# Performance work log

Hardware: AMD Instinct MI355X
Metric: run time of the kernel (lower is better)

The kernel has to match this reference:

```python
import jax, jax.numpy as jnp
import numpy as np

B, C, H, W = 2, 192, 128, 128
NUM_HEADS = 6
AMP = 1
NUM_OFFSETS = 9


def bilinear_sample(img, grid):
    # img: (C, H, W); grid: (Hn, Wn, 2) in [-1,1], align_corners=True, zeros padding
    Hh, Ww = img.shape[1], img.shape[2]
    x = (grid[..., 0] + 1.0) * 0.5 * (Ww - 1)
    y = (grid[..., 1] + 1.0) * 0.5 * (Hh - 1)
    x0 = jnp.floor(x)
    y0 = jnp.floor(y)
    x1 = x0 + 1.0
    y1 = y0 + 1.0
    wx1 = x - x0
    wy1 = y - y0

    def gather(yi, xi):
        valid = ((xi >= 0) & (xi <= Ww - 1) & (yi >= 0) & (yi <= Hh - 1)).astype(img.dtype)
        xc = jnp.clip(xi, 0, Ww - 1).astype(jnp.int32)
        yc = jnp.clip(yi, 0, Hh - 1).astype(jnp.int32)
        return img[:, yc, xc] * valid  # (C, Hn, Wn)

    return (gather(y0, x0) * ((1 - wy1) * (1 - wx1))
            + gather(y0, x1) * ((1 - wy1) * wx1)
            + gather(y1, x0) * (wy1 * (1 - wx1))
            + gather(y1, x1) * (wy1 * wx1))


def setup_inputs() -> dict:
    key = jax.random.key(0)
    ks = jax.random.split(key, 8)
    s = 0.02
    Ch = C // NUM_HEADS
    return {
        "x_q": jax.random.normal(ks[0], (B, C, H, W), jnp.float32),
        "x_kv": jax.random.normal(ks[1], (B, C, H, W), jnp.float32),
        "w_q": jax.random.normal(ks[2], (C, C), jnp.float32) * s,
        "w_kv": jax.random.normal(ks[3], (2 * C, C), jnp.float32) * s,
        "w_off1": jax.random.normal(ks[4], (C, 2 * C, 3, 3), jnp.float32) * s,
        "b_off1": jnp.zeros((C,), jnp.float32),
        "w_off2": jax.random.normal(ks[5], (2 * NUM_OFFSETS, C), jnp.float32) * s,
        "b_off2": jnp.zeros((2 * NUM_OFFSETS,), jnp.float32),
        "w_proj": jax.random.normal(ks[6], (C, C), jnp.float32) * s,
        "b_proj": jnp.zeros((C,), jnp.float32),
    }


def reference(x_q, x_kv, w_q, w_kv, w_off1, b_off1, w_off2, b_off2, w_proj, b_proj):
    Ch = C // NUM_HEADS
    scale = Ch ** (-0.5)

    # 1x1 conv projections as channel matmuls
    q = jnp.einsum('oc,bchw->bohw', w_q, x_q) * scale
    kv = jnp.einsum('oc,bchw->bohw', w_kv, x_kv)
    k, v = kv[:, :C], kv[:, C:]  # kv.reshape(B,2,Ch,nh,H,W) -> first C channels are k

    # offset predictor: 3x3 conv -> relu -> 1x1 conv
    off_in = jnp.concatenate([x_q, x_kv], axis=1)
    h1 = jax.lax.conv_general_dilated(off_in, w_off1, (1, 1), 'SAME',
                                      dimension_numbers=('NCHW', 'OIHW', 'NCHW'))
    h1 = jax.nn.relu(h1 + b_off1[None, :, None, None])
    off = jnp.einsum('oc,bchw->bohw', w_off2, h1) + b_off2[None, :, None, None]
    off = off.reshape(B, NUM_OFFSETS, 2, H, W).transpose(0, 1, 3, 4, 2)  # (B,9,H,W,2)
    gx = off[..., 0] / (W - 1) * 2.0 - 1.0
    gy = off[..., 1] / (H - 1) * 2.0 - 1.0
    grid = jnp.stack([gx, gy], axis=-1)  # (B,9,H,W,2)

    # deformable gather: sample full-channel k/v at each of 9 per-pixel offset grids
    sample = jax.vmap(jax.vmap(bilinear_sample, in_axes=(None, 0)), in_axes=(0, 0))
    k_s = sample(k, grid).reshape(B, NUM_OFFSETS, Ch, NUM_HEADS, H, W)
    v_s = sample(v, grid).reshape(B, NUM_OFFSETS, Ch, NUM_HEADS, H, W)

    q = q.reshape(B, Ch, NUM_HEADS, H, W)

    pad = [(0, 0), (0, 0), (0, 0), (0, 0), (AMP, AMP), (AMP, AMP)]
    k_p = jnp.pad(k_s, pad)
    v_p = jnp.pad(v_s, pad)

    win = 2 * AMP + 1
    logits = []
    for i in range(win):
        for j in range(win):
            idx = i * win + j
            kp = k_p[:, idx, :, :, i:i + H, j:j + W]  # (B,Ch,nh,H,W)
            logits.append(jnp.einsum('bchxy,bchxy->bhxy', q, kp))
    attn = jax.nn.softmax(jnp.stack(logits, axis=1), axis=1)  # (B,9,nh,H,W)

    out = jnp.zeros((B, Ch, NUM_HEADS, H, W), x_q.dtype)
    for i in range(win):
        for j in range(win):
            idx = i * win + j
            vp = v_p[:, idx, :, :, i:i + H, j:j + W]
            out = out + attn[:, idx, None] * vp

    out = out.reshape(B, C, H, W)  # channel layout = (Ch, nh), matching torch reshape
    return jnp.einsum('oc,bchw->bohw', w_proj, out) + b_proj[None, :, None, None]
```

## Files before the change

### kernel.cpp

```cpp
#include <hip/hip_runtime.h>
#include <math.h>

#define HW 16384
#define NB 2
#define NC 192

typedef __attribute__((ext_vector_type(8))) short bh8;
typedef __attribute__((ext_vector_type(4))) float f32x4;

__device__ inline ushort f2bf(float f) {
  union { float f; unsigned int u; } x; x.f = f;
  unsigned int r = x.u + 0x7fffu + ((x.u >> 16) & 1u);
  return (ushort)(r >> 16);
}
__device__ inline float bf2f(ushort u) {
  union { unsigned int i; float f; } x; x.i = ((unsigned int)u) << 16;
  return x.f;
}
__device__ inline float asf(unsigned int u) {
  union { unsigned int i; float f; } x; x.i = u; return x.f;
}
__device__ inline unsigned int cvtpk(float lo, float hi) {
  unsigned int r;
  asm("v_cvt_pk_bf16_f32 %0, %1, %2" : "=v"(r) : "v"(lo), "v"(hi));
  return r;
}
__device__ inline void gl16(const ushort* g, char* l) {
  __builtin_amdgcn_global_load_lds(
      (const __attribute__((address_space(1))) unsigned int*)g,
      (__attribute__((address_space(3))) unsigned int*)l, 16, 0, 0);
}

__global__ void k_wpack(const float* __restrict__ w1, ushort* __restrict__ wpack) {
  int i = blockIdx.x * 256 + threadIdx.x;
  int s = i / 6144;
  int rem = i - s * 6144;
  int o = rem >> 5, kk = rem & 31;
  int dy = s / 36, t2 = s - dy * 36;
  int icc = t2 / 3, dxi = t2 - icc * 3;
  int ic = icc * 32 + kk;
  wpack[i] = f2bf(w1[(size_t)o * 3456 + (size_t)ic * 9 + dy * 3 + dxi]);
}

__global__ void k_wgpack(const float* __restrict__ wq, const float* __restrict__ wkv,
                         const float* __restrict__ wp, float scale,
                         ushort* __restrict__ wg) {
  int i = blockIdx.x * 256 + threadIdx.x;
  int r = i / NC, c = i - r * NC;
  float v;
  if (r < 192) {
    int orow = (r & 31) * 6 + (r >> 5);
    v = wq[(size_t)orow * NC + c] * scale;
  } else if (r < 576) {
    int rp = r - 192;
    int t = rp >= 192 ? 1 : 0;
    int cc = rp - t * 192;
    int orow = t * 192 + (cc & 31) * 6 + (cc >> 5);
    v = wkv[(size_t)orow * NC + c];
  } else {
    int rp = r - 576;
    v = wp[(size_t)rp * NC + ((c & 31) * 6 + (c >> 5))];
  }
  wg[i] = f2bf(v);
}

__global__ void k_zero(uint4* __restrict__ p) {
  p[(size_t)blockIdx.x * 256 + threadIdx.x] = make_uint4(0u, 0u, 0u, 0u);
}

__global__ __launch_bounds__(256) void k_xpack(const float* __restrict__ xq,
                                               const float* __restrict__ xkv,
                                               ushort* __restrict__ xpp) {
  __shared__ float t[NC][65];
  const int tid = threadIdx.x;
  const size_t r0 = (size_t)blockIdx.x * 64;
  const int b = (int)(r0 >> 14);
  const int px0 = (int)(r0 & 16383);
  const int y = px0 >> 7, x0 = px0 & 127;
  const float* src = (blockIdx.y == 0 ? xq : xkv) + (size_t)b * NC * HW + px0;
#pragma unroll
  for (int it = 0; it < 12; ++it) {
    int i = it * 256 + tid;
    int c = i >> 4, q4 = i & 15;
    float4 v = *(const float4*)(src + (size_t)c * HW + q4 * 4);
    t[c][q4 * 4 + 0] = v.x; t[c][q4 * 4 + 1] = v.y;
    t[c][q4 * 4 + 2] = v.z; t[c][q4 * 4 + 3] = v.w;
  }
  __syncthreads();
  ushort* dst = xpp + ((size_t)(b * 130 + y + 1) * 132 + x0 + 1) * 384 +
                blockIdx.y * 192;
#pragma unroll
  for (int it = 0; it < 6; ++it) {
    int i = it * 256 + tid;
    int px = i / 24, ch = i - px * 24;
    ushort4 u0, u1;
    u0.x = f2bf(t[ch * 8 + 0][px]); u0.y = f2bf(t[ch * 8 + 1][px]);
    u0.z = f2bf(t[ch * 8 + 2][px]); u0.w = f2bf(t[ch * 8 + 3][px]);
    u1.x = f2bf(t[ch * 8 + 4][px]); u1.y = f2bf(t[ch * 8 + 5][px]);
    u1.z = f2bf(t[ch * 8 + 6][px]); u1.w = f2bf(t[ch * 8 + 7][px]);
    *(ushort4*)&dst[(size_t)px * 384 + ch * 8] = u0;
    *(ushort4*)&dst[(size_t)px * 384 + ch * 8 + 4] = u1;
  }
}

__device__ inline void stage64(ushort* lds, const ushort* src, int rowStride,
                               int tid) {
#pragma unroll
  for (int it = 0; it < 6; ++it) {
    int i = it * 256 + tid;
    int row = i / 24, c = i - row * 24;
    int pos = (c & 24) | ((c & 7) ^ (row & 7));
    uint4 v = *(const uint4*)(src + (size_t)row * rowStride + c * 8);
    *(uint4*)&lds[row * NC + pos * 8] = v;
  }
}
__device__ inline bh8 frag64(const ushort* lds, int row, int c) {
  int pos = (c & 24) | ((c & 7) ^ (row & 7));
  return *(const bh8*)&lds[row * NC + pos * 8];
}

__global__ __launch_bounds__(256) void k_gemm_mfma(
    const ushort* __restrict__ xpp, int cOff, const ushort* __restrict__ wg,
    ushort* __restrict__ outA, ushort* __restrict__ outB) {
  __shared__ __attribute__((aligned(16))) ushort xs[64 * NC];
  __shared__ __attribute__((aligned(16))) ushort ws2[64 * NC];
  const int tid = threadIdx.x;
  const size_t p0 = (size_t)blockIdx.x * 64;
  const int bb = (int)(p0 >> 14);
  const int yy = (int)((p0 >> 7) & 127);
  const int xx0 = (int)(p0 & 127);
  const int o0 = blockIdx.y * 64;
  const ushort* src = xpp + ((size_t)(bb * 130 + yy + 1) * 132 + xx0 + 1) * 384 + cOff;
  stage64(xs, src, 384, tid);
  stage64(ws2, wg + (size_t)o0 * NC, NC, tid);
  __syncthreads();
  const int lid = tid & 15, g = (tid >> 4) & 3, wv = tid >> 6;
  const int wo = (wv & 1) * 32, wp = (wv >> 1) * 32;
  f32x4 acc[2][2];
#pragma unroll
  for (int m = 0; m < 2; ++m)
#pragma unroll
    for (int n = 0; n < 2; ++n) acc[m][n] = (f32x4){0.f, 0.f, 0.f, 0.f};
#pragma unroll
  for (int k = 0; k < 6; ++k) {
    bh8 a0 = frag64(ws2, wo + lid, k * 4 + g);
    bh8 a1 = frag64(ws2, wo + 16 + lid, k * 4 + g);
    bh8 b0 = frag64(xs, wp + lid, k * 4 + g);
    bh8 b1 = frag64(xs, wp + 16 + lid, k * 4 + g);
    acc[0][0] = __builtin_amdgcn_mfma_f32_16x16x32_bf16(a0, b0, acc[0][0], 0, 0, 0);
    acc[0][1] = __builtin_amdgcn_mfma_f32_16x16x32_bf16(a0, b1, acc[0][1], 0, 0, 0);
    acc[1][0] = __builtin_amdgcn_mfma_f32_16x16x32_bf16(a1, b0, acc[1][0], 0, 0, 0);
    acc[1][1] = __builtin_amdgcn_mfma_f32_16x16x32_bf16(a1, b1, acc[1][1], 0, 0, 0);
  }
  const int t = o0 >= 192 ? 1 : 0;
  ushort* dst = t ? outB : outA;
  const int od = o0 - t * 192;
#pragma unroll
  for (int m = 0; m < 2; ++m)
#pragma unroll
    for (int n = 0; n < 2; ++n) {
      int orow = od + wo + m * 16 + g * 4;
      size_t px = p0 + wp + n * 16 + lid;
      ushort4 u;
      u.x = f2bf(acc[m][n][0]); u.y = f2bf(acc[m][n][1]);
      u.z = f2bf(acc[m][n][2]); u.w = f2bf(acc[m][n][3]);
      *(ushort4*)&dst[px * NC + orow] = u;
    }
}

__global__ __launch_bounds__(256) void k_proj_mfma(
    const ushort* __restrict__ pre, const ushort* __restrict__ wg,
    const float* __restrict__ bp, float* __restrict__ out) {
  __shared__ __attribute__((aligned(16))) ushort xs[64 * NC];
  __shared__ __attribute__((aligned(16))) ushort ws2[64 * NC];
  const int tid = threadIdx.x;
  const size_t p0 = (size_t)blockIdx.x * 64;
  const int o0 = blockIdx.y * 64;
  stage64(xs, pre + p0 * NC, NC, tid);
  stage64(ws2, wg + (size_t)o0 * NC, NC, tid);
  __syncthreads();
  const int lid = tid & 15, g = (tid >> 4) & 3, wv = tid >> 6;
  const int wo = (wv & 1) * 32, wp = (wv >> 1) * 32;
  f32x4 acc[2][2];
#pragma unroll
  for (int m = 0; m < 2; ++m)
#pragma unroll
    for (int n = 0; n < 2; ++n) acc[m][n] = (f32x4){0.f, 0.f, 0.f, 0.f};
#pragma unroll
  for (int k = 0; k < 6; ++k) {
    bh8 a0 = frag64(ws2, wo + lid, k * 4 + g);
    bh8 a1 = frag64(ws2, wo + 16 + lid, k * 4 + g);
    bh8 b0 = frag64(xs, wp + lid, k * 4 + g);
    bh8 b1 = frag64(xs, wp + 16 + lid, k * 4 + g);
    acc[0][0] = __builtin_amdgcn_mfma_f32_16x16x32_bf16(a0, b0, acc[0][0], 0, 0, 0);
    acc[0][1] = __builtin_amdgcn_mfma_f32_16x16x32_bf16(a0, b1, acc[0][1], 0, 0, 0);
    acc[1][0] = __builtin_amdgcn_mfma_f32_16x16x32_bf16(a1, b0, acc[1][0], 0, 0, 0);
    acc[1][1] = __builtin_amdgcn_mfma_f32_16x16x32_bf16(a1, b1, acc[1][1], 0, 0, 0);
  }
#pragma unroll
  for (int m = 0; m < 2; ++m)
#pragma unroll
    for (int n = 0; n < 2; ++n) {
      int oc = o0 + wo + m * 16 + g * 4;
      size_t pxf = p0 + wp + n * 16 + lid;
      int b = (int)(pxf >> 14);
      int px = (int)(pxf & 16383);
#pragma unroll
      for (int j = 0; j < 4; ++j)
        out[((size_t)b * NC + oc + j) * HW + px] = acc[m][n][j] + bp[oc + j];
    }
}

#define CP0 0
#define CP1 8448
#define CW0 16896
#define CW1 35328
__global__ __launch_bounds__(256, 3) void k_conv_mfma(
    const ushort* __restrict__ xpp, const ushort* __restrict__ wpack,
    const float* __restrict__ b1, ushort* __restrict__ h1) {
  __shared__ __attribute__((aligned(16))) char smem[53760];
  const int tid = threadIdx.x;
  const int bi = blockIdx.x;
  const int b = bi >> 8;
  const int y = (bi >> 1) & 127;
  const int oh = bi & 1;
  const int lid = tid & 15;
  const int g = (tid >> 4) & 3;
  const int wv = tid >> 6;
  const int lane = tid & 63;
  const int og = wv & 1;
  const int pg = wv >> 1;
  f32x4 acc[3][4];
#pragma unroll
  for (int m = 0; m < 3; ++m)
#pragma unroll
    for (int n = 0; n < 4; ++n) acc[m][n] = (f32x4){0.f, 0.f, 0.f, 0.f};

  auto stageP = [&](int icc, int dy, int buf) {
    const size_t rowbase = (size_t)(b * 130 + y + dy) * 132 * 384 + icc * 32;
    char* dst0 = smem + (buf ? CP1 : CP0);
    for (int grp = wv; grp < 9; grp += 4) {
      int i = grp * 64 + lane;
      if (i < 528) {
        int slot = i >> 2, ch = i & 3;
        gl16(xpp + rowbase + (size_t)slot * 384 + ((ch ^ ((slot >> 1) & 3)) << 3),
             dst0 + grp * 1024);
      }
    }
  };
  auto stageW = [&](int icc, int dy, int buf) {
    const ushort* wsrc = wpack + (size_t)((dy * 12 + icc) * 3) * 6144 + oh * 96 * 32;
    char* dst0 = smem + (buf ? CW1 : CW0);
    for (int grp = wv; grp < 18; grp += 4) {
      int i = grp * 64 + lane;
      int dxi = i / 384;
      int rem = i - dxi * 384;
      int o = rem >> 2, q = rem & 3;
      gl16(wsrc + (size_t)dxi * 6144 + o * 32 + ((q ^ ((o >> 1) & 3)) << 3),
           dst0 + grp * 1024);
    }
  };

  stageP(0, 0, 0);
  stageW(0, 0, 0);
  __syncthreads();
  int cur = 0;
  for (int s = 0; s < 36; ++s) {
    if (s < 35) {
      const int ns = s + 1;
      const int nicc = ns / 3, ndy = ns - nicc * 3;
      stageP(nicc, ndy, cur ^ 1);
      stageW(nicc, ndy, cur ^ 1);
    }
    const char* Pb = smem + (cur ? CP1 : CP0);
    const char* Wb = smem + (cur ? CW1 : CW0);
#pragma unroll
    for (int dxi = 0; dxi < 3; ++dxi) {
      bh8 af[3];
#pragma unroll
      for (int m = 0; m < 3; ++m) {
        int o = og * 48 + m * 16 + lid;
        af[m] = *(const bh8*)(Wb + ((dxi * 96 + o) << 6) +
                              ((g ^ ((o >> 1) & 3)) << 4));
      }
#pragma unroll
      for (int n = 0; n < 4; ++n) {
        int slot = pg * 64 + n * 16 + lid + dxi;
        bh8 bf = *(const bh8*)(Pb + (slot << 6) + ((g ^ ((slot >> 1) & 3)) << 4));
#pragma unroll
        for (int m = 0; m < 3; ++m)
          acc[m][n] = __builtin_amdgcn_mfma_f32_16x16x32_bf16(
              af[m], bf, acc[m][n], 0, 0, 0);
      }
    }
    __syncthreads();
    cur ^= 1;
  }

  const size_t pxbase = (size_t)(b << 14) + y * 128 + pg * 64;
#pragma unroll
  for (int m = 0; m < 3; ++m) {
    const int ob = oh * 96 + og * 48 + m * 16 + g * 4;
    float4 bv = *(const float4*)(b1 + ob);
#pragma unroll
    for (int n = 0; n < 4; ++n) {
      size_t px = pxbase + n * 16 + lid;
      h1[(size_t)(ob + 0) * (NB * HW) + px] = f2bf(fmaxf(acc[m][n][0] + bv.x, 0.f));
      h1[(size_t)(ob + 1) * (NB * HW) + px] = f2bf(fmaxf(acc[m][n][1] + bv.y, 0.f));
      h1[(size_t)(ob + 2) * (NB * HW) + px] = f2bf(fmaxf(acc[m][n][2] + bv.z, 0.f));
      h1[(size_t)(ob + 3) * (NB * HW) + px] = f2bf(fmaxf(acc[m][n][3] + bv.w, 0.f));
    }
  }
}

__global__ __launch_bounds__(256) void k_offhead(
    const ushort* __restrict__ h1, const float* __restrict__ w2,
    const float* __restrict__ b2, float* __restrict__ off) {
  __shared__ float w2l[18 * NC];
  const int tid = threadIdx.x;
  for (int i = tid; i < 18 * NC; i += 256) w2l[i] = w2[i];
  __syncthreads();
  const int px = tid & 127;
  const int jh = tid >> 7;
  const size_t p = (size_t)blockIdx.x * 128 + px;
  float acc[9];
#pragma unroll
  for (int jj = 0; jj < 9; ++jj) acc[jj] = b2[jh * 9 + jj];
  for (int c = 0; c < NC; ++c) {
    float v = bf2f(h1[(size_t)c * (NB * HW) + p]);
#pragma unroll
    for (int jj = 0; jj < 9; ++jj) acc[jj] += w2l[(jh * 9 + jj) * NC + c] * v;
  }
#pragma unroll
  for (int jj = 0; jj < 9; ++jj) off[p * 18 + jh * 9 + jj] = acc[jj];
}

__global__ __launch_bounds__(192, 8) void k_attn(
    const ushort* __restrict__ q, const ushort* __restrict__ k,
    const ushort* __restrict__ v, const float* __restrict__ off,
    ushort* __restrict__ pre) {
  const int s = threadIdx.x;
  const int pix = s / 48;
  const int sub = s - pix * 48;
  const size_t p = (size_t)blockIdx.x * 4 + pix;
  const int b = (int)(p >> 14);
  const int pp = (int)(p & 16383);
  const int y = pp >> 7, x = pp & 127;

  uint2 qu = *(const uint2*)(q + p * NC + 4 * sub);
  const float q0 = asf(qu.x << 16), q1 = asf(qu.x & 0xffff0000u);
  const float q2 = asf(qu.y << 16), q3 = asf(qu.y & 0xffff0000u);
  const size_t cbase = (size_t)b * HW * NC + 4 * sub;
  const size_t obase = (size_t)b * HW;

  float pl[9];
  unsigned int vp0[9], vp1[9];
#pragma unroll
  for (int idx = 0; idx < 9; ++idx) {
    const int yy = y + idx / 3 - 1, xx = x + idx % 3 - 1;
    const bool inb = (yy >= 0) && (yy < 128) && (xx >= 0) && (xx < 128);
    float sx = 0.f, sy = 0.f;
    if (inb) {
      const size_t sp = obase + yy * 128 + xx;
      sx = off[sp * 18 + idx * 2 + 0];
      sy = off[sp * 18 + idx * 2 + 1];
    }
    const float fx0 = floorf(sx), fy0 = floorf(sy);
    const float wx1 = sx - fx0, wy1 = sy - fy0;
    const float wx0 = 1.f - wx1, wy0 = 1.f - wy1;
    const float inbf = inb ? 1.f : 0.f;
    const float mx0 = (fx0 >= 0.f && fx0 <= 127.f) ? inbf : 0.f;
    const float mx1 = (fx0 >= -1.f && fx0 <= 126.f) ? inbf : 0.f;
    const float my0 = (fy0 >= 0.f && fy0 <= 127.f) ? 1.f : 0.f;
    const float my1 = (fy0 >= -1.f && fy0 <= 126.f) ? 1.f : 0.f;
    const int ix0 = (int)fminf(fmaxf(fx0, 0.f), 127.f);
    const int iy0 = (int)fminf(fmaxf(fy0, 0.f), 127.f);
    const int ix1 = (int)fminf(fmaxf(fx0 + 1.f, 0.f), 127.f);
    const int iy1 = (int)fminf(fmaxf(fy0 + 1.f, 0.f), 127.f);
    const float w00 = wy0 * wx0 * my0 * mx0, w01 = wy0 * wx1 * my0 * mx1;
    const float w10 = wy1 * wx0 * my1 * mx0, w11 = wy1 * wx1 * my1 * mx1;
    const size_t e00 = cbase + (size_t)(iy0 * 128 + ix0) * NC;
    const size_t e01 = cbase + (size_t)(iy0 * 128 + ix1) * NC;
    const size_t e10 = cbase + (size_t)(iy1 * 128 + ix0) * NC;
    const size_t e11 = cbase + (size_t)(iy1 * 128 + ix1) * NC;
    float ks0 = 0.f, ks1 = 0.f, ks2 = 0.f, ks3 = 0.f;
    float vs0 = 0.f, vs1 = 0.f, vs2 = 0.f, vs3 = 0.f;
#define CORNER(W, E)                                            \
  {                                                             \
    uint2 kk = *(const uint2*)(k + (E));                        \
    uint2 vvv = *(const uint2*)(v + (E));                       \
    ks0 = fmaf((W), asf(kk.x << 16), ks0);                      \
    ks1 = fmaf((W), asf(kk.x & 0xffff0000u), ks1);              \
    ks2 = fmaf((W), asf(kk.y << 16), ks2);                      \
    ks3 = fmaf((W), asf(kk.y & 0xffff0000u), ks3);              \
    vs0 = fmaf((W), asf(vvv.x << 16), vs0);                     \
    vs1 = fmaf((W), asf(vvv.x & 0xffff0000u), vs1);             \
    vs2 = fmaf((W), asf(vvv.y << 16), vs2);                     \
    vs3 = fmaf((W), asf(vvv.y & 0xffff0000u), vs3);             \
  }
    CORNER(w00, e00)
    CORNER(w01, e01)
    CORNER(w10, e10)
    CORNER(w11, e11)
#undef CORNER
    float pd = q0 * ks0 + q1 * ks1 + q2 * ks2 + q3 * ks3;
    pd += __shfl_xor(pd, 1);
    pd += __shfl_xor(pd, 2);
    pd += __shfl_xor(pd, 4);
    pl[idx] = pd;
    vp0[idx] = cvtpk(vs0, vs1);
    vp1[idx] = cvtpk(vs2, vs3);
  }
  float mx = pl[0];
#pragma unroll
  for (int i = 1; i < 9; ++i) mx = fmaxf(mx, pl[i]);
  float sm = 0.f;
#pragma unroll
  for (int i = 0; i < 9; ++i) { pl[i] = __expf(pl[i] - mx); sm += pl[i]; }
  const float inv = __builtin_amdgcn_rcpf(sm);
  float o0 = 0.f, o1 = 0.f, o2 = 0.f, o3 = 0.f;
#pragma unroll
  for (int i = 0; i < 9; ++i) {
    const float a = pl[i] * inv;
    o0 = fmaf(a, asf(vp0[i] << 16), o0);
    o1 = fmaf(a, asf(vp0[i] & 0xffff0000u), o1);
    o2 = fmaf(a, asf(vp1[i] << 16), o2);
    o3 = fmaf(a, asf(vp1[i] & 0xffff0000u), o3);
  }
  ushort4 r;
  r.x = f2bf(o0); r.y = f2bf(o1); r.z = f2bf(o2); r.w = f2bf(o3);
  *(ushort4*)(pre + p * NC + 4 * sub) = r;
}

extern "C" void kernel_launch(void* const* d_in, const int* in_sizes, int n_in,
                              void* d_out, int out_size, void* d_ws, size_t ws_size,
                              hipStream_t stream) {
  const float* x_q    = (const float*)d_in[0];
  const float* x_kv   = (const float*)d_in[1];
  const float* w_q    = (const float*)d_in[2];
  const float* w_kv   = (const float*)d_in[3];
  const float* w_off1 = (const float*)d_in[4];
  const float* b_off1 = (const float*)d_in[5];
  const float* w_off2 = (const float*)d_in[6];
  const float* b_off2 = (const float*)d_in[7];
  const float* w_proj = (const float*)d_in[8];
  const float* b_proj = (const float*)d_in[9];
  float* out = (float*)d_out;

  char* W = (char*)d_ws;
  const size_t SB = (size_t)NB * HW * NC * 2;
  ushort* qb   = (ushort*)W;
  ushort* kb   = (ushort*)(W + SB);
  ushort* vb   = (ushort*)(W + 2 * SB);
  ushort* preb = (ushort*)(W + 3 * SB);
  ushort* h1b  = preb;
  ushort* wg   = (ushort*)(W + 4 * SB);
  ushort* xpp  = (ushort*)(W + 4 * SB + 294912);
  float*  offb = (float*)xpp;
  ushort* wpk  = (ushort*)d_out;

  const float scale = 0.17677669529663687f;
  dim3 blk(256);
  k_wpack<<<dim3(2592), blk, 0, stream>>>(w_off1, wpk);
  k_wgpack<<<dim3(576), blk, 0, stream>>>(w_q, w_kv, w_proj, scale, wg);
  k_zero<<<dim3(6435), blk, 0, stream>>>((uint4*)xpp);
  k_xpack<<<dim3(512, 2), blk, 0, stream>>>(x_q, x_kv, xpp);
  k_gemm_mfma<<<dim3(512, 3), blk, 0, stream>>>(xpp, 0, wg, qb, qb);
  k_gemm_mfma<<<dim3(512, 6), blk, 0, stream>>>(xpp, 192, wg + 192 * NC, kb, vb);
  k_conv_mfma<<<dim3(512), blk, 0, stream>>>(xpp, wpk, b_off1, h1b);
  k_offhead<<<dim3(NB * 128), blk, 0, stream>>>(h1b, w_off2, b_off2, offb);
  k_attn<<<dim3(8192), dim3(192), 0, stream>>>(qb, kb, vb, offb, preb);
  k_proj_mfma<<<dim3(512, 3), blk, 0, stream>>>(preb, wg + 576 * NC, b_proj, out);
}
```

Measured before the change: 194.8 us.

## Merge q/k/v projection GEMMs and use bf16 dot2 with 32-bit offsets in attention

The two projection GEMM launches become one, where each block stages its activation tile once and loops over three 64-row weight tiles to produce all 192 output channels of q, k or v. This cuts repeated activation staging and one launch, but leaves fewer, longer blocks (1536 instead of 4608). The attention kernel now folds the q·k product into each bilinear corner with v_dot2_f32_bf16 instead of accumulating four k channels first, and uses 32-bit address arithmetic. Both changes aim to reduce ALU and address work, at the cost of a slightly different rounding order for the logits.

```diff
diff --git a/kernel.cpp b/kernel.cpp
--- a/kernel.cpp
+++ b/kernel.cpp
@@ -120,8 +120,8 @@
 }
 
 __global__ __launch_bounds__(256) void k_gemm_mfma(
-    const ushort* __restrict__ xpp, int cOff, const ushort* __restrict__ wg,
-    ushort* __restrict__ outA, ushort* __restrict__ outB) {
+    const ushort* __restrict__ xpp, const ushort* __restrict__ wg,
+    ushort* __restrict__ qb, ushort* __restrict__ kb, ushort* __restrict__ vb) {
   __shared__ __attribute__((aligned(16))) ushort xs[64 * NC];
   __shared__ __attribute__((aligned(16))) ushort ws2[64 * NC];
   const int tid = threadIdx.x;
@@ -129,43 +129,47 @@
   const int bb = (int)(p0 >> 14);
   const int yy = (int)((p0 >> 7) & 127);
   const int xx0 = (int)(p0 & 127);
-  const int o0 = blockIdx.y * 64;
+  const int which = blockIdx.y;
+  const int cOff = (which == 0) ? 0 : 192;
   const ushort* src = xpp + ((size_t)(bb * 130 + yy + 1) * 132 + xx0 + 1) * 384 + cOff;
+  const ushort* wbase = wg + (size_t)(which * 192) * NC;
+  ushort* dst = which == 0 ? qb : (which == 1 ? kb : vb);
   stage64(xs, src, 384, tid);
-  stage64(ws2, wg + (size_t)o0 * NC, NC, tid);
-  __syncthreads();
   const int lid = tid & 15, g = (tid >> 4) & 3, wv = tid >> 6;
   const int wo = (wv & 1) * 32, wp = (wv >> 1) * 32;
-  f32x4 acc[2][2];
-#pragma unroll
-  for (int m = 0; m < 2; ++m)
-#pragma unroll
-    for (int n = 0; n < 2; ++n) acc[m][n] = (f32x4){0.f, 0.f, 0.f, 0.f};
-#pragma unroll
-  for (int k = 0; k < 6; ++k) {
-    bh8 a0 = frag64(ws2, wo + lid, k * 4 + g);
-    bh8 a1 = frag64(ws2, wo + 16 + lid, k * 4 + g);
-    bh8 b0 = frag64(xs, wp + lid, k * 4 + g);
-    bh8 b1 = frag64(xs, wp + 16 + lid, k * 4 + g);
-    acc[0][0] = __builtin_amdgcn_mfma_f32_16x16x32_bf16(a0, b0, acc[0][0], 0, 0, 0);
-    acc[0][1] = __builtin_amdgcn_mfma_f32_16x16x32_bf16(a0, b1, acc[0][1], 0, 0, 0);
-    acc[1][0] = __builtin_amdgcn_mfma_f32_16x16x32_bf16(a1, b0, acc[1][0], 0, 0, 0);
-    acc[1][1] = __builtin_amdgcn_mfma_f32_16x16x32_bf16(a1, b1, acc[1][1], 0, 0, 0);
-  }
-  const int t = o0 >= 192 ? 1 : 0;
-  ushort* dst = t ? outB : outA;
-  const int od = o0 - t * 192;
-#pragma unroll
-  for (int m = 0; m < 2; ++m)
-#pragma unroll
-    for (int n = 0; n < 2; ++n) {
-      int orow = od + wo + m * 16 + g * 4;
-      size_t px = p0 + wp + n * 16 + lid;
-      ushort4 u;
-      u.x = f2bf(acc[m][n][0]); u.y = f2bf(acc[m][n][1]);
-      u.z = f2bf(acc[m][n][2]); u.w = f2bf(acc[m][n][3]);
-      *(ushort4*)&dst[px * NC + orow] = u;
-    }
+  for (int ot = 0; ot < 3; ++ot) {
+    if (ot) __syncthreads();
+    stage64(ws2, wbase + (size_t)(ot * 64) * NC, NC, tid);
+    __syncthreads();
+    f32x4 acc[2][2];
+#pragma unroll
+    for (int m = 0; m < 2; ++m)
+#pragma unroll
+      for (int n = 0; n < 2; ++n) acc[m][n] = (f32x4){0.f, 0.f, 0.f, 0.f};
+#pragma unroll
+    for (int k = 0; k < 6; ++k) {
+      bh8 a0 = frag64(ws2, wo + lid, k * 4 + g);
+      bh8 a1 = frag64(ws2, wo + 16 + lid, k * 4 + g);
+      bh8 b0 = frag64(xs, wp + lid, k * 4 + g);
+      bh8 b1 = frag64(xs, wp + 16 + lid, k * 4 + g);
+      acc[0][0] = __builtin_amdgcn_mfma_f32_16x16x32_bf16(a0, b0, acc[0][0], 0, 0, 0);
+      acc[0][1] = __builtin_amdgcn_mfma_f32_16x16x32_bf16(a0, b1, acc[0][1], 0, 0, 0);
+      acc[1][0] = __builtin_amdgcn_mfma_f32_16x16x32_bf16(a1, b0, acc[1][0], 0, 0, 0);
+      acc[1][1] = __builtin_amdgcn_mfma_f32_16x16x32_bf16(a1, b1, acc[1][1], 0, 0, 0);
+    }
+    const int od = ot * 64;
+#pragma unroll
+    for (int m = 0; m < 2; ++m)
+#pragma unroll
+      for (int n = 0; n < 2; ++n) {
+        int orow = od + wo + m * 16 + g * 4;
+        size_t px = p0 + wp + n * 16 + lid;
+        ushort4 u;
+        u.x = f2bf(acc[m][n][0]); u.y = f2bf(acc[m][n][1]);
+        u.z = f2bf(acc[m][n][2]); u.w = f2bf(acc[m][n][3]);
+        *(ushort4*)&dst[px * NC + orow] = u;
+      }
+  }
 }
 
 __global__ __launch_bounds__(256) void k_proj_mfma(
@@ -342,16 +346,15 @@
   const int s = threadIdx.x;
   const int pix = s / 48;
   const int sub = s - pix * 48;
-  const size_t p = (size_t)blockIdx.x * 4 + pix;
-  const int b = (int)(p >> 14);
-  const int pp = (int)(p & 16383);
+  const int p = blockIdx.x * 4 + pix;
+  const int b = p >> 14;
+  const int pp = p & 16383;
   const int y = pp >> 7, x = pp & 127;
 
-  uint2 qu = *(const uint2*)(q + p * NC + 4 * sub);
-  const float q0 = asf(qu.x << 16), q1 = asf(qu.x & 0xffff0000u);
-  const float q2 = asf(qu.y << 16), q3 = asf(qu.y & 0xffff0000u);
-  const size_t cbase = (size_t)b * HW * NC + 4 * sub;
-  const size_t obase = (size_t)b * HW;
+  uint2 qu = *(const uint2*)(q + (size_t)p * NC + 4 * sub);
+  const unsigned int cbase = (unsigned int)b * (HW * NC) + 4 * sub;
+  const int obase = b * HW;
+  const float fz = 0.f;
 
   float pl[9];
   unsigned int vp0[9], vp1[9];
@@ -361,7 +364,7 @@
     const bool inb = (yy >= 0) && (yy < 128) && (xx >= 0) && (xx < 128);
     float sx = 0.f, sy = 0.f;
     if (inb) {
-      const size_t sp = obase + yy * 128 + xx;
+      const int sp = obase + yy * 128 + xx;
       sx = off[sp * 18 + idx * 2 + 0];
       sy = off[sp * 18 + idx * 2 + 1];
     }
@@ -369,41 +372,42 @@
     const float wx1 = sx - fx0, wy1 = sy - fy0;
     const float wx0 = 1.f - wx1, wy0 = 1.f - wy1;
     const float inbf = inb ? 1.f : 0.f;
-    const float mx0 = (fx0 >= 0.f && fx0 <= 127.f) ? inbf : 0.f;
-    const float mx1 = (fx0 >= -1.f && fx0 <= 126.f) ? inbf : 0.f;
-    const float my0 = (fy0 >= 0.f && fy0 <= 127.f) ? 1.f : 0.f;
-    const float my1 = (fy0 >= -1.f && fy0 <= 126.f) ? 1.f : 0.f;
+    const float wxm0 = wx0 * ((fx0 >= 0.f && fx0 <= 127.f) ? inbf : 0.f);
+    const float wxm1 = wx1 * ((fx0 >= -1.f && fx0 <= 126.f) ? inbf : 0.f);
+    const float wym0 = wy0 * ((fy0 >= 0.f && fy0 <= 127.f) ? 1.f : 0.f);
+    const float wym1 = wy1 * ((fy0 >= -1.f && fy0 <= 126.f) ? 1.f : 0.f);
     const int ix0 = (int)fminf(fmaxf(fx0, 0.f), 127.f);
     const int iy0 = (int)fminf(fmaxf(fy0, 0.f), 127.f);
     const int ix1 = (int)fminf(fmaxf(fx0 + 1.f, 0.f), 127.f);
     const int iy1 = (int)fminf(fmaxf(fy0 + 1.f, 0.f), 127.f);
-    const float w00 = wy0 * wx0 * my0 * mx0, w01 = wy0 * wx1 * my0 * mx1;
-    const float w10 = wy1 * wx0 * my1 * mx0, w11 = wy1 * wx1 * my1 * mx1;
-    const size_t e00 = cbase + (size_t)(iy0 * 128 + ix0) * NC;
-    const size_t e01 = cbase + (size_t)(iy0 * 128 + ix1) * NC;
-    const size_t e10 = cbase + (size_t)(iy1 * 128 + ix0) * NC;
-    const size_t e11 = cbase + (size_t)(iy1 * 128 + ix1) * NC;
-    float ks0 = 0.f, ks1 = 0.f, ks2 = 0.f, ks3 = 0.f;
+    const float w00 = wym0 * wxm0, w01 = wym0 * wxm1;
+    const float w10 = wym1 * wxm0, w11 = wym1 * wxm1;
+    const unsigned int e00 = cbase + (unsigned int)(iy0 * 128 + ix0) * 192u;
+    const unsigned int e01 = cbase + (unsigned int)(iy0 * 128 + ix1) * 192u;
+    const unsigned int e10 = cbase + (unsigned int)(iy1 * 128 + ix0) * 192u;
+    const unsigned int e11 = cbase + (unsigned int)(iy1 * 128 + ix1) * 192u;
+    float pd = 0.f;
     float vs0 = 0.f, vs1 = 0.f, vs2 = 0.f, vs3 = 0.f;
-#define CORNER(W, E)                                            \
-  {                                                             \
-    uint2 kk = *(const uint2*)(k + (E));                        \
-    uint2 vvv = *(const uint2*)(v + (E));                       \
-    ks0 = fmaf((W), asf(kk.x << 16), ks0);                      \
-    ks1 = fmaf((W), asf(kk.x & 0xffff0000u), ks1);              \
-    ks2 = fmaf((W), asf(kk.y << 16), ks2);                      \
-    ks3 = fmaf((W), asf(kk.y & 0xffff0000u), ks3);              \
-    vs0 = fmaf((W), asf(vvv.x << 16), vs0);                     \
-    vs1 = fmaf((W), asf(vvv.x & 0xffff0000u), vs1);             \
-    vs2 = fmaf((W), asf(vvv.y << 16), vs2);                     \
-    vs3 = fmaf((W), asf(vvv.y & 0xffff0000u), vs3);             \
+#define CORNER(W, E)                                              \
+  {                                                               \
+    uint2 kk = *(const uint2*)(k + (E));                          \
+    uint2 vv = *(const uint2*)(v + (E));                          \
+    float d0, d1;                                                 \
+    asm("v_dot2_f32_bf16 %0, %1, %2, %3"                          \
+        : "=v"(d0) : "v"(qu.x), "v"(kk.x), "v"(fz));              \
+    asm("v_dot2_f32_bf16 %0, %1, %2, %3"                          \
+        : "=v"(d1) : "v"(qu.y), "v"(kk.y), "v"(d0));              \
+    pd = fmaf((W), d1, pd);                                       \
+    vs0 = fmaf((W), asf(vv.x << 16), vs0);                        \
+    vs1 = fmaf((W), asf(vv.x & 0xffff0000u), vs1);                \
+    vs2 = fmaf((W), asf(vv.y << 16), vs2);                        \
+    vs3 = fmaf((W), asf(vv.y & 0xffff0000u), vs3);                \
   }
     CORNER(w00, e00)
     CORNER(w01, e01)
     CORNER(w10, e10)
     CORNER(w11, e11)
 #undef CORNER
-    float pd = q0 * ks0 + q1 * ks1 + q2 * ks2 + q3 * ks3;
     pd += __shfl_xor(pd, 1);
     pd += __shfl_xor(pd, 2);
     pd += __shfl_xor(pd, 4);
@@ -429,7 +433,7 @@
   }
   ushort4 r;
   r.x = f2bf(o0); r.y = f2bf(o1); r.z = f2bf(o2); r.w = f2bf(o3);
-  *(ushort4*)(pre + p * NC + 4 * sub) = r;
+  *(ushort4*)(pre + (size_t)p * NC + 4 * sub) = r;
 }
 
 extern "C" void kernel_launch(void* const* d_in, const int* in_sizes, int n_in,
@@ -465,8 +469,7 @@
   k_wgpack<<<dim3(576), blk, 0, stream>>>(w_q, w_kv, w_proj, scale, wg);
   k_zero<<<dim3(6435), blk, 0, stream>>>((uint4*)xpp);
   k_xpack<<<dim3(512, 2), blk, 0, stream>>>(x_q, x_kv, xpp);
-  k_gemm_mfma<<<dim3(512, 3), blk, 0, stream>>>(xpp, 0, wg, qb, qb);
-  k_gemm_mfma<<<dim3(512, 6), blk, 0, stream>>>(xpp, 192, wg + 192 * NC, kb, vb);
+  k_gemm_mfma<<<dim3(512, 3), blk, 0, stream>>>(xpp, wg, qb, kb, vb);
   k_conv_mfma<<<dim3(512), blk, 0, stream>>>(xpp, wpk, b_off1, h1b);
   k_offhead<<<dim3(NB * 128), blk, 0, stream>>>(h1b, w_off2, b_off2, offb);
   k_attn<<<dim3(8192), dim3(192), 0, stream>>>(qb, kb, vb, offb, preb);
```

After: 189.5 us. 2.7% less time.
